# Kernel optimization log

Measured on AMD Instinct MI355X. Metric: run time of the kernel, lower is better.

Reference implementation:

```python
import jax, jax.numpy as jnp
import numpy as np


def setup_inputs() -> dict:
    key = jax.random.key(0)
    k0, k1, k2, k3, k4 = jax.random.split(key, 5)
    B, S, H, I, E = 4, 2048, 1024, 3584, 8
    scale = 0.02
    return {
        "hidden_states": jax.random.normal(k0, (B, S, H), jnp.float32),
        "gate_w": jax.random.normal(k1, (E, H), jnp.float32) * scale,
        "Wg": jax.random.normal(k2, (E, I, H), jnp.float32) * scale,
        "Wu": jax.random.normal(k3, (E, I, H), jnp.float32) * scale,
        "Wd": jax.random.normal(k4, (E, H, I), jnp.float32) * scale,
        "top_k": 2,
    }


def reference(hidden_states, gate_w, Wg, Wu, Wd, top_k):
    B, S, H = hidden_states.shape
    E = gate_w.shape[0]
    x = hidden_states.reshape(-1, H)  # [N, H]

    # Router: softmax in float32 (matches torch dtype=torch.float), then top-k + renorm.
    router_logits = x @ gate_w.T  # [N, E]
    routing_probs = jax.nn.softmax(router_logits.astype(jnp.float32), axis=-1)
    top_w, sel = jax.lax.top_k(routing_probs, top_k)  # [N, K]
    top_w = top_w / jnp.sum(top_w, axis=-1, keepdims=True)
    top_w = top_w.astype(x.dtype)

    # Combined per-token weight for each expert: sum of top-k weights routed to it.
    # comb[n, e] = sum_k top_w[n, k] * (sel[n, k] == e)
    comb = jnp.einsum("nk,nke->ne", top_w, jax.nn.one_hot(sel, E, dtype=x.dtype))

    out = jnp.zeros_like(x)
    for e in range(E):  # fixed small loop over experts (structurally distinct weights)
        h = jax.nn.silu(x @ Wg[e].T) * (x @ Wu[e].T)  # [N, I] SwiGLU
        out = out + (h @ Wd[e].T) * comb[:, e:e + 1]
    return out.reshape(B, S, H), router_logits
```

## Files before the change

### kernel.cpp

```cpp
#include <hip/hip_runtime.h>
#include <hip/hip_bf16.h>

#define N_TOK 8192
#define H_DIM 1024
#define I_DIM 3584
#define N_EXP 8
#define N_PAIR (N_TOK * 2)

#define BM 128
#define BN 128
#define BK 32
#define MAX_TILES 144

#define NPAN1 (I_DIM / BN)
#define NPAN2 (H_DIM / BN)
#define NWG1  (MAX_TILES * NPAN1)
#define NWG2  (MAX_TILES * NPAN2)

typedef short bf16x8 __attribute__((ext_vector_type(8)));
typedef float f32x4 __attribute__((ext_vector_type(4)));

#define WS_CNT      0
#define WS_FILL     64
#define WS_OFF      128
#define WS_NTILES   192
#define WS_TILETAB  256
#define WS_SEL      2048
#define WS_WGT      (WS_SEL    + 2 * N_TOK * 4)
#define WS_PTOK     (WS_WGT    + 2 * N_TOK * 4)
#define WS_PW       (WS_PTOK   + N_PAIR * 4)
#define WS_XBF      (WS_PW     + N_PAIR * 4)
#define WS_HBUF     (WS_XBF    + (size_t)N_TOK * H_DIM * 2)
#define WBF_ELEMS   ((size_t)N_EXP * I_DIM * H_DIM)
#define WS_WGBF     (WS_HBUF + (size_t)N_PAIR * I_DIM * 2)
#define WS_WUBF     (WS_WGBF + WBF_ELEMS * 2)
#define WS_END      (WS_WUBF + WBF_ELEMS * 2)

__device__ __forceinline__ unsigned short f2bf(float f) {
  unsigned int u = __float_as_uint(f);
  unsigned int r = (u + 0x7fffu + ((u >> 16) & 1u)) >> 16;
  return (unsigned short)r;
}

__device__ __forceinline__ uint4 pack8(float4 a, float4 b) {
  uint4 r;
  r.x = (unsigned)f2bf(a.x) | ((unsigned)f2bf(a.y) << 16);
  r.y = (unsigned)f2bf(a.z) | ((unsigned)f2bf(a.w) << 16);
  r.z = (unsigned)f2bf(b.x) | ((unsigned)f2bf(b.y) << 16);
  r.w = (unsigned)f2bf(b.z) | ((unsigned)f2bf(b.w) << 16);
  return r;
}

__device__ __forceinline__ void gll16(const ushort* g, ushort* l) {
  __builtin_amdgcn_global_load_lds(
      (const __attribute__((address_space(1))) unsigned int*)g,
      (__attribute__((address_space(3))) unsigned int*)l, 16, 0, 0);
}

__global__ __launch_bounds__(64) void k_router(
    const float* __restrict__ x, const float* __restrict__ gw,
    float* __restrict__ logits, int* __restrict__ sel,
    float* __restrict__ wgt, int* __restrict__ cnt,
    ushort* __restrict__ xbf)
{
  const int n = blockIdx.x;
  const int lane = threadIdx.x;
  const float4* xr = (const float4*)(x + (size_t)n * H_DIM + lane * 16);
  float4 x0 = xr[0], x1 = xr[1], x2 = xr[2], x3 = xr[3];

  uint4* xo = (uint4*)(xbf + (size_t)n * H_DIM + lane * 16);
  xo[0] = pack8(x0, x1);
  xo[1] = pack8(x2, x3);

  float l[N_EXP];
#pragma unroll
  for (int e = 0; e < N_EXP; ++e) {
    const float4* wr = (const float4*)(gw + e * H_DIM + lane * 16);
    float4 w0 = wr[0], w1 = wr[1], w2 = wr[2], w3 = wr[3];
    float p = x0.x * w0.x + x0.y * w0.y + x0.z * w0.z + x0.w * w0.w
            + x1.x * w1.x + x1.y * w1.y + x1.z * w1.z + x1.w * w1.w
            + x2.x * w2.x + x2.y * w2.y + x2.z * w2.z + x2.w * w2.w
            + x3.x * w3.x + x3.y * w3.y + x3.z * w3.z + x3.w * w3.w;
#pragma unroll
    for (int o = 32; o >= 1; o >>= 1) p += __shfl_xor(p, o, 64);
    l[e] = p;
  }
  float m = l[0];
#pragma unroll
  for (int e = 1; e < N_EXP; ++e) m = fmaxf(m, l[e]);
  float pr[N_EXP]; float den = 0.f;
#pragma unroll
  for (int e = 0; e < N_EXP; ++e) { pr[e] = expf(l[e] - m); den += pr[e]; }
#pragma unroll
  for (int e = 0; e < N_EXP; ++e) pr[e] /= den;
  int i0 = 0; float p0 = pr[0];
#pragma unroll
  for (int e = 1; e < N_EXP; ++e) { if (pr[e] > p0) { p0 = pr[e]; i0 = e; } }
  int i1 = -1; float p1 = -1.f;
#pragma unroll
  for (int e = 0; e < N_EXP; ++e) { if (e != i0 && pr[e] > p1) { p1 = pr[e]; i1 = e; } }
  float rs = 1.f / (p0 + p1);
  if (lane == 0) {
    float* lo = logits + (size_t)n * N_EXP;
#pragma unroll
    for (int e = 0; e < N_EXP; ++e) lo[e] = l[e];
    sel[2 * n] = i0; sel[2 * n + 1] = i1;
    wgt[2 * n] = p0 * rs; wgt[2 * n + 1] = p1 * rs;
    atomicAdd(&cnt[i0], 1);
    atomicAdd(&cnt[i1], 1);
  }
}

__global__ void k_prefix(const int* __restrict__ cnt, int* __restrict__ off,
                         int* __restrict__ ntiles, int* __restrict__ tab)
{
  if (threadIdx.x != 0 || blockIdx.x != 0) return;
  int acc = 0, nt = 0;
  for (int e = 0; e < N_EXP; ++e) {
    off[e] = acc;
    int c = cnt[e];
    for (int r = 0; r < c; r += BM) {
      tab[nt * 3 + 0] = e;
      tab[nt * 3 + 1] = acc + r;
      tab[nt * 3 + 2] = (c - r < BM) ? (c - r) : BM;
      nt++;
    }
    acc += c;
  }
  off[N_EXP] = acc;
  *ntiles = nt;
}

__global__ __launch_bounds__(256) void k_scatter(
    const int* __restrict__ sel, const float* __restrict__ wgt,
    const int* __restrict__ off, int* __restrict__ fill,
    int* __restrict__ ptok, float* __restrict__ pw)
{
  int n = blockIdx.x * 256 + threadIdx.x;
  if (n >= N_TOK) return;
#pragma unroll
  for (int k = 0; k < 2; ++k) {
    int e = sel[2 * n + k];
    int pos = atomicAdd(&fill[e], 1);
    int row = off[e] + pos;
    ptok[row] = n;
    pw[row] = wgt[2 * n + k];
  }
}

__global__ __launch_bounds__(256) void k_cvtw(const float* __restrict__ src,
                                              ushort* __restrict__ dst)
{
  size_t i = (size_t)blockIdx.x * 256 + threadIdx.x;
  const float4* s = (const float4*)(src + i * 8);
  float4 a = s[0], b = s[1];
  ((uint4*)dst)[i] = pack8(a, b);
}


__global__ __launch_bounds__(256) void k_mlp1b(
    const ushort* __restrict__ Wg, const ushort* __restrict__ Wu,
    const ushort* __restrict__ xbf, const int* __restrict__ ptok,
    const int* __restrict__ ntiles, const int* __restrict__ tab,
    ushort* __restrict__ hbuf)
{
  __shared__ ushort sA[2][BM * BK];
  __shared__ ushort sG[2][BN * BK];
  __shared__ ushort sU[2][BN * BK];
  __shared__ int stok[BM];

  const int orig = blockIdx.x;
  const int lin = (orig & 7) * (NWG1 >> 3) + (orig >> 3);
  const int tile = lin / NPAN1;
  const int i0 = (lin % NPAN1) * BN;

  if (tile >= *ntiles) return;
  const int e = tab[tile * 3 + 0];
  const int row0 = tab[tile * 3 + 1];
  const int nrows = tab[tile * 3 + 2];
  const int t = threadIdx.x;

  if (t < BM) {
    int tt = t < nrows ? t : (nrows - 1);
    stok[t] = ptok[row0 + tt];
  }
  __syncthreads();

  const int ak = (t & 3) * 8;
  const ushort* ga0 = xbf + (size_t)stok[t >> 2] * H_DIM + ak;
  const ushort* ga1 = xbf + (size_t)stok[64 + (t >> 2)] * H_DIM + ak;

  const ushort* gg0 = Wg + (size_t)e * I_DIM * H_DIM + (size_t)(i0 + (t >> 2)) * H_DIM + ak;
  const ushort* gg1 = gg0 + (size_t)64 * H_DIM;
  const ushort* gu0 = Wu + (size_t)e * I_DIM * H_DIM + (size_t)(i0 + (t >> 2)) * H_DIM + ak;
  const ushort* gu1 = gu0 + (size_t)64 * H_DIM;

  const int lane = t & 63, wid = t >> 6;
  const int wm = wid >> 1, wn = wid & 1;
  const int fr = lane & 15, fq = lane >> 4;

  f32x4 ag[4][4], au[4][4];
#pragma unroll
  for (int m = 0; m < 4; ++m)
#pragma unroll
    for (int n = 0; n < 4; ++n) { ag[m][n] = (f32x4){0,0,0,0}; au[m][n] = (f32x4){0,0,0,0}; }

#define STAGE1(b, kt) do {                      \
    gll16(ga0 + (kt), &sA[b][t * 8]);           \
    gll16(ga1 + (kt), &sA[b][(256 + t) * 8]);   \
    gll16(gg0 + (kt), &sG[b][t * 8]);           \
    gll16(gg1 + (kt), &sG[b][(256 + t) * 8]);   \
    gll16(gu0 + (kt), &sU[b][t * 8]);           \
    gll16(gu1 + (kt), &sU[b][(256 + t) * 8]);   \
  } while (0)

#define COMPUTE1(b) do {                                                     \
    bf16x8 a[4], bg[4], bu[4];                                               \
    _Pragma("unroll")                                                        \
    for (int m = 0; m < 4; ++m)                                              \
      a[m] = *(const bf16x8*)(&sA[b][(wm * 64 + m * 16 + fr) * BK + fq * 8]);\
    _Pragma("unroll")                                                        \
    for (int n = 0; n < 4; ++n) {                                            \
      bg[n] = *(const bf16x8*)(&sG[b][(wn * 64 + n * 16 + fr) * BK + fq * 8]);\
      bu[n] = *(const bf16x8*)(&sU[b][(wn * 64 + n * 16 + fr) * BK + fq * 8]);\
    }                                                                        \
    _Pragma("unroll")                                                        \
    for (int m = 0; m < 4; ++m)                                              \
      _Pragma("unroll")                                                      \
      for (int n = 0; n < 4; ++n) {                                          \
        ag[m][n] = __builtin_amdgcn_mfma_f32_16x16x32_bf16(a[m], bg[n], ag[m][n], 0, 0, 0); \
        au[m][n] = __builtin_amdgcn_mfma_f32_16x16x32_bf16(a[m], bu[n], au[m][n], 0, 0, 0); \
      }                                                                      \
  } while (0)

  const int NK = H_DIM / BK;
  STAGE1(0, 0);
  __syncthreads();
  for (int ki = 0; ki < NK - 1; ++ki) {
    const int cur = ki & 1;
    STAGE1(cur ^ 1, (ki + 1) * BK);
    COMPUTE1(cur);
    __syncthreads();
  }
  COMPUTE1((NK - 1) & 1);
#undef STAGE1
#undef COMPUTE1

#pragma unroll
  for (int m = 0; m < 4; ++m) {
    const int rb = wm * 64 + m * 16 + fq * 4;
#pragma unroll
    for (int n = 0; n < 4; ++n) {
      const int col = i0 + wn * 64 + n * 16 + fr;
#pragma unroll
      for (int r = 0; r < 4; ++r) {
        const int row = rb + r;
        if (row < nrows) {
          float g = ag[m][n][r], u = au[m][n][r];
          float hv = (g / (1.f + __expf(-g))) * u;
          hbuf[(size_t)(row0 + row) * I_DIM + col] = f2bf(hv);
        }
      }
    }
  }
}

__global__ __launch_bounds__(256) void k_mlp2b(
    const ushort* __restrict__ Wd, const ushort* __restrict__ hbuf,
    const int* __restrict__ ptok, const float* __restrict__ pw,
    const int* __restrict__ ntiles, const int* __restrict__ tab,
    float* __restrict__ out)
{
  __shared__ ushort sA[2][BM * BK];
  __shared__ ushort sB[2][BN * BK];
  __shared__ int stok[BM];
  __shared__ float sw[BM];

  const int orig = blockIdx.x;
  const int lin = (orig & 7) * (NWG2 >> 3) + (orig >> 3);
  const int tile = lin / NPAN2;
  const int j0 = (lin % NPAN2) * BN;

  if (tile >= *ntiles) return;
  const int e = tab[tile * 3 + 0];
  const int row0 = tab[tile * 3 + 1];
  const int nrows = tab[tile * 3 + 2];
  const int t = threadIdx.x;

  if (t < BM) {
    int tt = t < nrows ? t : (nrows - 1);
    stok[t] = ptok[row0 + tt];
    sw[t] = pw[row0 + tt];
  }
  __syncthreads();

  const int ak = (t & 3) * 8;
  int arow0 = row0 + (t >> 2);       if (arow0 > N_PAIR - 1) arow0 = N_PAIR - 1;
  int arow1 = row0 + 64 + (t >> 2);  if (arow1 > N_PAIR - 1) arow1 = N_PAIR - 1;
  const ushort* ga0 = hbuf + (size_t)arow0 * I_DIM + ak;
  const ushort* ga1 = hbuf + (size_t)arow1 * I_DIM + ak;

  const ushort* gb0 = Wd + (size_t)e * H_DIM * I_DIM + (size_t)(j0 + (t >> 2)) * I_DIM + ak;
  const ushort* gb1 = gb0 + (size_t)64 * I_DIM;

  const int lane = t & 63, wid = t >> 6;
  const int wm = wid >> 1, wn = wid & 1;
  const int fr = lane & 15, fq = lane >> 4;

  f32x4 ac[4][4];
#pragma unroll
  for (int m = 0; m < 4; ++m)
#pragma unroll
    for (int n = 0; n < 4; ++n) ac[m][n] = (f32x4){0,0,0,0};

#define STAGE2(b, kt) do {                      \
    gll16(ga0 + (kt), &sA[b][t * 8]);           \
    gll16(ga1 + (kt), &sA[b][(256 + t) * 8]);   \
    gll16(gb0 + (kt), &sB[b][t * 8]);           \
    gll16(gb1 + (kt), &sB[b][(256 + t) * 8]);   \
  } while (0)

#define COMPUTE2(b) do {                                                     \
    bf16x8 a[4], bb[4];                                                      \
    _Pragma("unroll")                                                        \
    for (int m = 0; m < 4; ++m)                                              \
      a[m] = *(const bf16x8*)(&sA[b][(wm * 64 + m * 16 + fr) * BK + fq * 8]);\
    _Pragma("unroll")                                                        \
    for (int n = 0; n < 4; ++n)                                              \
      bb[n] = *(const bf16x8*)(&sB[b][(wn * 64 + n * 16 + fr) * BK + fq * 8]);\
    _Pragma("unroll")                                                        \
    for (int m = 0; m < 4; ++m)                                              \
      _Pragma("unroll")                                                      \
      for (int n = 0; n < 4; ++n)                                            \
        ac[m][n] = __builtin_amdgcn_mfma_f32_16x16x32_bf16(a[m], bb[n], ac[m][n], 0, 0, 0); \
  } while (0)

  const int NK = I_DIM / BK;
  STAGE2(0, 0);
  __syncthreads();
  for (int ki = 0; ki < NK - 1; ++ki) {
    const int cur = ki & 1;
    STAGE2(cur ^ 1, (ki + 1) * BK);
    COMPUTE2(cur);
    __syncthreads();
  }
  COMPUTE2((NK - 1) & 1);
#undef STAGE2
#undef COMPUTE2

#pragma unroll
  for (int m = 0; m < 4; ++m) {
    const int rb = wm * 64 + m * 16 + fq * 4;
#pragma unroll
    for (int n = 0; n < 4; ++n) {
      const int col = j0 + wn * 64 + n * 16 + fr;
#pragma unroll
      for (int r = 0; r < 4; ++r) {
        const int row = rb + r;
        if (row < nrows) {
          float v = ac[m][n][r] * sw[row];
          atomicAdd(&out[(size_t)stok[row] * H_DIM + col], v);
        }
      }
    }
  }
}


__global__ __launch_bounds__(256) void k_mlp1(
    const float* __restrict__ Wg, const float* __restrict__ Wu,
    const ushort* __restrict__ xbf, const int* __restrict__ ptok,
    const int* __restrict__ ntiles, const int* __restrict__ tab,
    ushort* __restrict__ hbuf)
{
  __shared__ ushort sA[BM * BK];
  __shared__ ushort sG[BN * BK];
  __shared__ ushort sU[BN * BK];
  __shared__ int stok[BM];

  const int tile = blockIdx.x;
  if (tile >= *ntiles) return;
  const int e = tab[tile * 3 + 0];
  const int row0 = tab[tile * 3 + 1];
  const int nrows = tab[tile * 3 + 2];
  const int i0 = blockIdx.y * BN;
  const int t = threadIdx.x;

  if (t < BM) {
    int tt = t < nrows ? t : (nrows - 1);
    stok[t] = ptok[row0 + tt];
  }
  __syncthreads();

  const int ak = (t & 3) * 8;
  const ushort* ga0 = xbf + (size_t)stok[t >> 2] * H_DIM + ak;
  const ushort* ga1 = xbf + (size_t)stok[64 + (t >> 2)] * H_DIM + ak;
  ushort* la0 = sA + (size_t)t * 8;
  ushort* la1 = sA + (size_t)(256 + t) * 8;

  const int wr = t >> 1, wcb = (t & 1) * 16;
  const float* gwg = Wg + (size_t)e * I_DIM * H_DIM + (size_t)(i0 + wr) * H_DIM + wcb;
  const float* gwu = Wu + (size_t)e * I_DIM * H_DIM + (size_t)(i0 + wr) * H_DIM + wcb;
  ushort* lwg = sG + wr * BK + wcb;
  ushort* lwu = sU + wr * BK + wcb;

  const int lane = t & 63, wid = t >> 6;
  const int wm = wid >> 1, wn = wid & 1;
  const int fr = lane & 15, fq = lane >> 4;

  f32x4 ag[4][4], au[4][4];
#pragma unroll
  for (int m = 0; m < 4; ++m)
#pragma unroll
    for (int n = 0; n < 4; ++n) { ag[m][n] = (f32x4){0,0,0,0}; au[m][n] = (f32x4){0,0,0,0}; }

  for (int kt = 0; kt < H_DIM; kt += BK) {
    gll16(ga0 + kt, la0);
    gll16(ga1 + kt, la1);

    const float4* pg = (const float4*)(gwg + kt);
    const float4* pu = (const float4*)(gwu + kt);
    float4 g0 = pg[0], g1 = pg[1], g2 = pg[2], g3 = pg[3];
    float4 u0 = pu[0], u1 = pu[1], u2 = pu[2], u3 = pu[3];
    ((uint4*)lwg)[0] = pack8(g0, g1);
    ((uint4*)lwg)[1] = pack8(g2, g3);
    ((uint4*)lwu)[0] = pack8(u0, u1);
    ((uint4*)lwu)[1] = pack8(u2, u3);
    __syncthreads();

    bf16x8 a[4], bg[4], bu[4];
#pragma unroll
    for (int m = 0; m < 4; ++m)
      a[m] = *(const bf16x8*)(sA + (wm * 64 + m * 16 + fr) * BK + fq * 8);
#pragma unroll
    for (int n = 0; n < 4; ++n) {
      bg[n] = *(const bf16x8*)(sG + (wn * 64 + n * 16 + fr) * BK + fq * 8);
      bu[n] = *(const bf16x8*)(sU + (wn * 64 + n * 16 + fr) * BK + fq * 8);
    }
#pragma unroll
    for (int m = 0; m < 4; ++m)
#pragma unroll
      for (int n = 0; n < 4; ++n) {
        ag[m][n] = __builtin_amdgcn_mfma_f32_16x16x32_bf16(a[m], bg[n], ag[m][n], 0, 0, 0);
        au[m][n] = __builtin_amdgcn_mfma_f32_16x16x32_bf16(a[m], bu[n], au[m][n], 0, 0, 0);
      }
    __syncthreads();
  }

#pragma unroll
  for (int m = 0; m < 4; ++m) {
    const int rb = wm * 64 + m * 16 + fq * 4;
#pragma unroll
    for (int n = 0; n < 4; ++n) {
      const int col = i0 + wn * 64 + n * 16 + fr;
#pragma unroll
      for (int r = 0; r < 4; ++r) {
        const int row = rb + r;
        if (row < nrows) {
          float g = ag[m][n][r], u = au[m][n][r];
          float hv = (g / (1.f + __expf(-g))) * u;
          hbuf[(size_t)(row0 + row) * I_DIM + col] = f2bf(hv);
        }
      }
    }
  }
}

__global__ __launch_bounds__(256) void k_mlp2(
    const float* __restrict__ Wd, const ushort* __restrict__ hbuf,
    const int* __restrict__ ptok, const float* __restrict__ pw,
    const int* __restrict__ ntiles, const int* __restrict__ tab,
    float* __restrict__ out)
{
  __shared__ ushort sA[BM * BK];
  __shared__ ushort sB[BN * BK];
  __shared__ int stok[BM];
  __shared__ float sw[BM];

  const int tile = blockIdx.x;
  if (tile >= *ntiles) return;
  const int e = tab[tile * 3 + 0];
  const int row0 = tab[tile * 3 + 1];
  const int nrows = tab[tile * 3 + 2];
  const int j0 = blockIdx.y * BN;
  const int t = threadIdx.x;

  if (t < BM) {
    int tt = t < nrows ? t : (nrows - 1);
    stok[t] = ptok[row0 + tt];
    sw[t] = pw[row0 + tt];
  }
  __syncthreads();

  const int ak = (t & 3) * 8;
  int arow0 = row0 + (t >> 2);       if (arow0 > N_PAIR - 1) arow0 = N_PAIR - 1;
  int arow1 = row0 + 64 + (t >> 2);  if (arow1 > N_PAIR - 1) arow1 = N_PAIR - 1;
  const ushort* ga0 = hbuf + (size_t)arow0 * I_DIM + ak;
  const ushort* ga1 = hbuf + (size_t)arow1 * I_DIM + ak;
  ushort* la0 = sA + (size_t)t * 8;
  ushort* la1 = sA + (size_t)(256 + t) * 8;

  const int wr = t >> 1, wcb = (t & 1) * 16;
  const float* gb = Wd + (size_t)e * H_DIM * I_DIM + (size_t)(j0 + wr) * I_DIM + wcb;
  ushort* lb = sB + wr * BK + wcb;

  const int lane = t & 63, wid = t >> 6;
  const int wm = wid >> 1, wn = wid & 1;
  const int fr = lane & 15, fq = lane >> 4;

  f32x4 ac[4][4];
#pragma unroll
  for (int m = 0; m < 4; ++m)
#pragma unroll
    for (int n = 0; n < 4; ++n) ac[m][n] = (f32x4){0,0,0,0};

  for (int kt = 0; kt < I_DIM; kt += BK) {
    gll16(ga0 + kt, la0);
    gll16(ga1 + kt, la1);

    const float4* pb = (const float4*)(gb + kt);
    float4 b0 = pb[0], b1 = pb[1], b2 = pb[2], b3 = pb[3];
    ((uint4*)lb)[0] = pack8(b0, b1);
    ((uint4*)lb)[1] = pack8(b2, b3);
    __syncthreads();

    bf16x8 a[4], bb[4];
#pragma unroll
    for (int m = 0; m < 4; ++m)
      a[m] = *(const bf16x8*)(sA + (wm * 64 + m * 16 + fr) * BK + fq * 8);
#pragma unroll
    for (int n = 0; n < 4; ++n)
      bb[n] = *(const bf16x8*)(sB + (wn * 64 + n * 16 + fr) * BK + fq * 8);
#pragma unroll
    for (int m = 0; m < 4; ++m)
#pragma unroll
      for (int n = 0; n < 4; ++n)
        ac[m][n] = __builtin_amdgcn_mfma_f32_16x16x32_bf16(a[m], bb[n], ac[m][n], 0, 0, 0);
    __syncthreads();
  }

#pragma unroll
  for (int m = 0; m < 4; ++m) {
    const int rb = wm * 64 + m * 16 + fq * 4;
#pragma unroll
    for (int n = 0; n < 4; ++n) {
      const int col = j0 + wn * 64 + n * 16 + fr;
#pragma unroll
      for (int r = 0; r < 4; ++r) {
        const int row = rb + r;
        if (row < nrows) {
          float v = ac[m][n][r] * sw[row];
          atomicAdd(&out[(size_t)stok[row] * H_DIM + col], v);
        }
      }
    }
  }
}

extern "C" void kernel_launch(void* const* d_in, const int* in_sizes, int n_in,
                              void* d_out, int out_size, void* d_ws, size_t ws_size,
                              hipStream_t stream)
{
  const float* x  = (const float*)d_in[0];
  const float* gw = (const float*)d_in[1];
  const float* Wg = (const float*)d_in[2];
  const float* Wu = (const float*)d_in[3];
  const float* Wd = (const float*)d_in[4];

  float* out    = (float*)d_out;
  float* logits = out + (size_t)N_TOK * H_DIM;

  char* ws = (char*)d_ws;
  int*    cnt    = (int*)(ws + WS_CNT);
  int*    fill   = (int*)(ws + WS_FILL);
  int*    off    = (int*)(ws + WS_OFF);
  int*    ntiles = (int*)(ws + WS_NTILES);
  int*    tab    = (int*)(ws + WS_TILETAB);
  int*    sel    = (int*)(ws + WS_SEL);
  float*  wgt    = (float*)(ws + WS_WGT);
  int*    ptok   = (int*)(ws + WS_PTOK);
  float*  pw     = (float*)(ws + WS_PW);
  ushort* xbf    = (ushort*)(ws + WS_XBF);
  ushort* hbuf   = (ushort*)(ws + WS_HBUF);
  ushort* wgbf   = (ushort*)(ws + WS_WGBF);
  ushort* wubf   = (ushort*)(ws + WS_WUBF);
  ushort* wdbf   = wgbf;

  const bool fast = (ws_size >= WS_END);

  hipMemsetAsync(d_out, 0, (size_t)N_TOK * H_DIM * sizeof(float), stream);
  hipMemsetAsync(ws, 0, 128, stream);

  k_router<<<N_TOK, 64, 0, stream>>>(x, gw, logits, sel, wgt, cnt, xbf);
  k_prefix<<<1, 64, 0, stream>>>(cnt, off, ntiles, tab);
  k_scatter<<<N_TOK / 256, 256, 0, stream>>>(sel, wgt, off, fill, ptok, pw);

  const int cvtblocks = (int)(WBF_ELEMS / 8 / 256);

  if (fast) {
    k_cvtw<<<cvtblocks, 256, 0, stream>>>(Wg, wgbf);
    k_cvtw<<<cvtblocks, 256, 0, stream>>>(Wu, wubf);
    k_mlp1b<<<NWG1, 256, 0, stream>>>(wgbf, wubf, xbf, ptok, ntiles, tab, hbuf);
    k_cvtw<<<cvtblocks, 256, 0, stream>>>(Wd, wdbf);
    k_mlp2b<<<NWG2, 256, 0, stream>>>(wdbf, hbuf, ptok, pw, ntiles, tab, out);
  } else {
    dim3 gA(MAX_TILES, I_DIM / BN);
    dim3 gB(MAX_TILES, H_DIM / BN);
    k_mlp1<<<gA, 256, 0, stream>>>(Wg, Wu, xbf, ptok, ntiles, tab, hbuf);
    k_mlp2<<<gB, 256, 0, stream>>>(Wd, hbuf, ptok, pw, ntiles, tab, out);
  }
}
```

Measured before the change: 1.009 ms.

## Double row tile to 256 with 512-thread workgroups in expert GEMMs

Raises the per-expert row tile from 128 to 256 and launches 512-thread workgroups for the bf16 MFMA kernels, so each weight tile loaded from memory is reused across twice as many token rows. This halves the number of tiles and the total weight traffic. The fallback fp32 kernels keep a 128-row tile by splitting each 256-row tile across a grid z dimension. The trade-off is more LDS and registers per workgroup, fewer workgroups, and more padding waste on partially filled expert tiles. The warp mapping shown (wm = wid>>1 over 8 waves) must cover the 256 rows for the result to be correct.

```diff
diff --git a/kernel.cpp b/kernel.cpp
--- a/kernel.cpp
+++ b/kernel.cpp
@@ -7,10 +7,10 @@
 #define N_EXP 8
 #define N_PAIR (N_TOK * 2)
 
-#define BM 128
+#define BM 256
 #define BN 128
 #define BK 32
-#define MAX_TILES 144
+#define MAX_TILES 72
 
 #define NPAN1 (I_DIM / BN)
 #define NPAN2 (H_DIM / BN)
@@ -158,7 +158,7 @@
 }
 
 
-__global__ __launch_bounds__(256) void k_mlp1b(
+__global__ __launch_bounds__(512) void k_mlp1b(
     const ushort* __restrict__ Wg, const ushort* __restrict__ Wu,
     const ushort* __restrict__ xbf, const int* __restrict__ ptok,
     const int* __restrict__ ntiles, const int* __restrict__ tab,
@@ -187,13 +187,12 @@
   __syncthreads();
 
   const int ak = (t & 3) * 8;
-  const ushort* ga0 = xbf + (size_t)stok[t >> 2] * H_DIM + ak;
-  const ushort* ga1 = xbf + (size_t)stok[64 + (t >> 2)] * H_DIM + ak;
-
-  const ushort* gg0 = Wg + (size_t)e * I_DIM * H_DIM + (size_t)(i0 + (t >> 2)) * H_DIM + ak;
-  const ushort* gg1 = gg0 + (size_t)64 * H_DIM;
-  const ushort* gu0 = Wu + (size_t)e * I_DIM * H_DIM + (size_t)(i0 + (t >> 2)) * H_DIM + ak;
-  const ushort* gu1 = gu0 + (size_t)64 * H_DIM;
+  const int ar = t >> 2;
+  const ushort* ga0 = xbf + (size_t)stok[ar] * H_DIM + ak;
+  const ushort* ga1 = xbf + (size_t)stok[128 + ar] * H_DIM + ak;
+
+  const ushort* gg0 = Wg + (size_t)e * I_DIM * H_DIM + (size_t)(i0 + ar) * H_DIM + ak;
+  const ushort* gu0 = Wu + (size_t)e * I_DIM * H_DIM + (size_t)(i0 + ar) * H_DIM + ak;
 
   const int lane = t & 63, wid = t >> 6;
   const int wm = wid >> 1, wn = wid & 1;
@@ -207,11 +206,9 @@
 
 #define STAGE1(b, kt) do {                      \
     gll16(ga0 + (kt), &sA[b][t * 8]);           \
-    gll16(ga1 + (kt), &sA[b][(256 + t) * 8]);   \
+    gll16(ga1 + (kt), &sA[b][(512 + t) * 8]);   \
     gll16(gg0 + (kt), &sG[b][t * 8]);           \
-    gll16(gg1 + (kt), &sG[b][(256 + t) * 8]);   \
     gll16(gu0 + (kt), &sU[b][t * 8]);           \
-    gll16(gu1 + (kt), &sU[b][(256 + t) * 8]);   \
   } while (0)
 
 #define COMPUTE1(b) do {                                                     \
@@ -265,7 +262,7 @@
   }
 }
 
-__global__ __launch_bounds__(256) void k_mlp2b(
+__global__ __launch_bounds__(512) void k_mlp2b(
     const ushort* __restrict__ Wd, const ushort* __restrict__ hbuf,
     const int* __restrict__ ptok, const float* __restrict__ pw,
     const int* __restrict__ ntiles, const int* __restrict__ tab,
@@ -295,13 +292,13 @@
   __syncthreads();
 
   const int ak = (t & 3) * 8;
-  int arow0 = row0 + (t >> 2);       if (arow0 > N_PAIR - 1) arow0 = N_PAIR - 1;
-  int arow1 = row0 + 64 + (t >> 2);  if (arow1 > N_PAIR - 1) arow1 = N_PAIR - 1;
+  const int ar = t >> 2;
+  int arow0 = row0 + ar;        if (arow0 > N_PAIR - 1) arow0 = N_PAIR - 1;
+  int arow1 = row0 + 128 + ar;  if (arow1 > N_PAIR - 1) arow1 = N_PAIR - 1;
   const ushort* ga0 = hbuf + (size_t)arow0 * I_DIM + ak;
   const ushort* ga1 = hbuf + (size_t)arow1 * I_DIM + ak;
 
-  const ushort* gb0 = Wd + (size_t)e * H_DIM * I_DIM + (size_t)(j0 + (t >> 2)) * I_DIM + ak;
-  const ushort* gb1 = gb0 + (size_t)64 * I_DIM;
+  const ushort* gb0 = Wd + (size_t)e * H_DIM * I_DIM + (size_t)(j0 + ar) * I_DIM + ak;
 
   const int lane = t & 63, wid = t >> 6;
   const int wm = wid >> 1, wn = wid & 1;
@@ -315,9 +312,8 @@
 
 #define STAGE2(b, kt) do {                      \
     gll16(ga0 + (kt), &sA[b][t * 8]);           \
-    gll16(ga1 + (kt), &sA[b][(256 + t) * 8]);   \
+    gll16(ga1 + (kt), &sA[b][(512 + t) * 8]);   \
     gll16(gb0 + (kt), &sB[b][t * 8]);           \
-    gll16(gb1 + (kt), &sB[b][(256 + t) * 8]);   \
   } while (0)
 
 #define COMPUTE2(b) do {                                                     \
@@ -367,26 +363,30 @@
 }
 
 
+#define FBM 128
+
 __global__ __launch_bounds__(256) void k_mlp1(
     const float* __restrict__ Wg, const float* __restrict__ Wu,
     const ushort* __restrict__ xbf, const int* __restrict__ ptok,
     const int* __restrict__ ntiles, const int* __restrict__ tab,
     ushort* __restrict__ hbuf)
 {
-  __shared__ ushort sA[BM * BK];
+  __shared__ ushort sA[FBM * BK];
   __shared__ ushort sG[BN * BK];
   __shared__ ushort sU[BN * BK];
-  __shared__ int stok[BM];
+  __shared__ int stok[FBM];
 
   const int tile = blockIdx.x;
   if (tile >= *ntiles) return;
   const int e = tab[tile * 3 + 0];
-  const int row0 = tab[tile * 3 + 1];
-  const int nrows = tab[tile * 3 + 2];
+  const int row0 = tab[tile * 3 + 1] + (blockIdx.z ? FBM : 0);
+  int nrows = tab[tile * 3 + 2] - (blockIdx.z ? FBM : 0);
+  if (nrows <= 0) return;
+  if (nrows > FBM) nrows = FBM;
   const int i0 = blockIdx.y * BN;
   const int t = threadIdx.x;
 
-  if (t < BM) {
+  if (t < FBM) {
     int tt = t < nrows ? t : (nrows - 1);
     stok[t] = ptok[row0 + tt];
   }
@@ -472,20 +472,22 @@
     const int* __restrict__ ntiles, const int* __restrict__ tab,
     float* __restrict__ out)
 {
-  __shared__ ushort sA[BM * BK];
+  __shared__ ushort sA[FBM * BK];
   __shared__ ushort sB[BN * BK];
-  __shared__ int stok[BM];
-  __shared__ float sw[BM];
+  __shared__ int stok[FBM];
+  __shared__ float sw[FBM];
 
   const int tile = blockIdx.x;
   if (tile >= *ntiles) return;
   const int e = tab[tile * 3 + 0];
-  const int row0 = tab[tile * 3 + 1];
-  const int nrows = tab[tile * 3 + 2];
+  const int row0 = tab[tile * 3 + 1] + (blockIdx.z ? FBM : 0);
+  int nrows = tab[tile * 3 + 2] - (blockIdx.z ? FBM : 0);
+  if (nrows <= 0) return;
+  if (nrows > FBM) nrows = FBM;
   const int j0 = blockIdx.y * BN;
   const int t = threadIdx.x;
 
-  if (t < BM) {
+  if (t < FBM) {
     int tt = t < nrows ? t : (nrows - 1);
     stok[t] = ptok[row0 + tt];
     sw[t] = pw[row0 + tt];
@@ -600,12 +602,12 @@
   if (fast) {
     k_cvtw<<<cvtblocks, 256, 0, stream>>>(Wg, wgbf);
     k_cvtw<<<cvtblocks, 256, 0, stream>>>(Wu, wubf);
-    k_mlp1b<<<NWG1, 256, 0, stream>>>(wgbf, wubf, xbf, ptok, ntiles, tab, hbuf);
+    k_mlp1b<<<NWG1, 512, 0, stream>>>(wgbf, wubf, xbf, ptok, ntiles, tab, hbuf);
     k_cvtw<<<cvtblocks, 256, 0, stream>>>(Wd, wdbf);
-    k_mlp2b<<<NWG2, 256, 0, stream>>>(wdbf, hbuf, ptok, pw, ntiles, tab, out);
+    k_mlp2b<<<NWG2, 512, 0, stream>>>(wdbf, hbuf, ptok, pw, ntiles, tab, out);
   } else {
-    dim3 gA(MAX_TILES, I_DIM / BN);
-    dim3 gB(MAX_TILES, H_DIM / BN);
+    dim3 gA(MAX_TILES, I_DIM / BN, 2);
+    dim3 gB(MAX_TILES, H_DIM / BN, 2);
     k_mlp1<<<gA, 256, 0, stream>>>(Wg, Wu, xbf, ptok, ntiles, tab, hbuf);
     k_mlp2<<<gB, 256, 0, stream>>>(Wd, hbuf, ptok, pw, ntiles, tab, out);
   }
```

New measurement: 985.1 us. 2.4% less time.
